# Kernel optimization log

Hardware: AMD Instinct MI355X
Metric: run time of the kernel (lower is better)

Reference implementation:

```python
import jax, jax.numpy as jnp
import numpy as np

N = 100000      # nodes
E = 6400000     # edges
F_IN = 128      # input feature dim (lazily inferred by PyG)
C = 2           # out_channels (hard-coded in module)
NEG_SLOPE = 0.2 # GATConv default leaky_relu slope


def setup_inputs() -> dict:
    key = jax.random.key(0)
    ks = jax.random.split(key, 8)
    x = jax.random.normal(ks[0], (N, F_IN), dtype=jnp.float32)
    edge_index = jax.random.randint(ks[1], (2, E), 0, N, dtype=jnp.int64)
    edge_attr = jax.random.normal(ks[2], (E, 1), dtype=jnp.float32)
    s = 1.0 / np.sqrt(F_IN)
    W_src = (jax.random.normal(ks[3], (F_IN, C), dtype=jnp.float32) * s)
    W_edge = jax.random.normal(ks[4], (1, C), dtype=jnp.float32)
    att_src = jax.random.normal(ks[5], (C,), dtype=jnp.float32)
    att_dst = jax.random.normal(ks[6], (C,), dtype=jnp.float32)
    att_edge = jax.random.normal(ks[7], (C,), dtype=jnp.float32)
    bias = jnp.zeros((C,), dtype=jnp.float32)
    return {"x": x, "edge_index": edge_index, "edge_attr": edge_attr,
            "W_src": W_src, "W_edge": W_edge, "att_src": att_src,
            "att_dst": att_dst, "att_edge": att_edge, "bias": bias}


def reference(x, edge_index, edge_attr, W_src, W_edge, att_src, att_dst, att_edge, bias):
    src, dst = edge_index[0], edge_index[1]
    # Single-tensor input in PyG GATConv -> x_src = x_dst = lin_src(x)
    h = x @ W_src                      # [N, C]  (heads=1 folded away)
    a_src = h @ att_src                # [N]
    a_dst = h @ att_dst                # [N]
    he = edge_attr @ W_edge            # [E, C]
    a_e = he @ att_edge                # [E]
    # per-edge attention logit
    alpha = a_src[src] + a_dst[dst] + a_e
    alpha = jax.nn.leaky_relu(alpha, NEG_SLOPE)
    # segment softmax over incoming edges of each destination node
    amax = jax.ops.segment_max(alpha, dst, num_segments=N)
    amax = jnp.where(jnp.isfinite(amax), amax, 0.0)  # empty segments
    ex = jnp.exp(alpha - amax[dst])
    denom = jax.ops.segment_sum(ex, dst, num_segments=N)
    alpha_n = ex / (denom[dst] + 1e-16)
    # weighted scatter-add aggregation
    msg = h[src] * alpha_n[:, None]    # [E, C]
    out = jax.ops.segment_sum(msg, dst, num_segments=N) + bias  # [N, C]
    return out, alpha_n[:, None]       # alpha: [E, heads=1]
```

## Files before the change

### kernel.cpp

```cpp
#include <hip/hip_runtime.h>
#include <hip/hip_fp16.h>

#define NN 100000
#define NE 6400000
#define NEG_SLOPE 0.2f

#define NBIN 32
#define BSLICE 3125
#define NCH 16
#define ABLK 512
#define EPB (NE / ABLK)
#define RND 4096
#define CAP 256
#define SROW 257
#define NODEBLK 1024

#define FSLICE 10240
#define FNSLICE 10
#define FNCHUNK 20
#define FCHUNK (NE / FNCHUNK)

__global__ void gat_node_hist(const float* __restrict__ x, const float* __restrict__ W,
                              const float* __restrict__ att_src, const float* __restrict__ att_dst,
                              uint2* __restrict__ pack8, float* __restrict__ asrc,
                              float* __restrict__ adst,
                              const int* __restrict__ dst, int* __restrict__ cnt) {
    if (blockIdx.x < NODEBLK) {
        int gtid = blockIdx.x * 256 + threadIdx.x;
        int wave = gtid >> 6, lane = threadIdx.x & 63;
        const int nw = (NODEBLK * 256) >> 6;
        float as0 = att_src[0], as1 = att_src[1];
        float ad0 = att_dst[0], ad1 = att_dst[1];
        for (int node = wave; node < NN; node += nw) {
            float2 xx = *(const float2*)(x + (size_t)node * 128 + lane * 2);
            float2 w0 = *(const float2*)(W + lane * 4);
            float2 w1 = *(const float2*)(W + lane * 4 + 2);
            float c0 = xx.x * w0.x + xx.y * w1.x;
            float c1 = xx.x * w0.y + xx.y * w1.y;
            #pragma unroll
            for (int off = 32; off; off >>= 1) {
                c0 += __shfl_down(c0, off);
                c1 += __shfl_down(c1, off);
            }
            if (lane == 0) {
                float s = c0 * as0 + c1 * as1;
                float d = c0 * ad0 + c1 * ad1;
                unsigned h01 = (unsigned)__half_as_ushort(__float2half_rn(c0)) |
                               ((unsigned)__half_as_ushort(__float2half_rn(c1)) << 16);
                pack8[node] = make_uint2(h01, __float_as_uint(s));
                asrc[node] = s;
                adst[node] = d;
            }
        }
    } else {
        __shared__ unsigned h[NBIN];
        const int ablk = blockIdx.x - NODEBLK, t = threadIdx.x;
        if (t < NBIN) h[t] = 0;
        __syncthreads();
        const int b0 = ablk * EPB;
        for (int o = t * 4; o < EPB; o += 1024) {
            int4 d4 = *(const int4*)(dst + b0 + o);
            const int* dp = (const int*)&d4;
            #pragma unroll
            for (int u = 0; u < 4; ++u)
                atomicAdd(&h[(unsigned)dp[u] / BSLICE], 1u);
        }
        __syncthreads();
        if (t < NBIN) cnt[t * ABLK + ablk] = (int)h[t];
    }
}

__global__ __launch_bounds__(1024) void
gat_prefix(int* __restrict__ cnt, int* __restrict__ binstart) {
    __shared__ int btot[NBIN];
    __shared__ int bst[NBIN + 1];
    const int t = threadIdx.x, w = t >> 6, l = t & 63;
    int c[2][8], s[2], incl[2];
    #pragma unroll
    for (int q = 0; q < 2; ++q) {
        const int b = w + q * 16;
        int* row = cnt + b * ABLK;
        int ss = 0;
        #pragma unroll
        for (int j = 0; j < 8; ++j) { c[q][j] = row[l * 8 + j]; ss += c[q][j]; }
        int inc = ss;
        #pragma unroll
        for (int d = 1; d < 64; d <<= 1) {
            int v = __shfl_up(inc, d);
            if (l >= d) inc += v;
        }
        if (l == 63) btot[b] = inc;
        s[q] = ss; incl[q] = inc;
    }
    __syncthreads();
    if (t == 0) {
        int run = 0;
        for (int b = 0; b < NBIN; ++b) { bst[b] = run; run += btot[b]; }
        bst[NBIN] = run;
    }
    __syncthreads();
    #pragma unroll
    for (int q = 0; q < 2; ++q) {
        const int b = w + q * 16;
        int* row = cnt + b * ABLK;
        int base = bst[b] + incl[q] - s[q];
        #pragma unroll
        for (int j = 0; j < 8; ++j) { row[l * 8 + j] = base; base += c[q][j]; }
    }
    if (t <= NBIN) binstart[t] = bst[t];
}

__global__ __launch_bounds__(1024) void
gat_scatter(const int* __restrict__ src, const int* __restrict__ dst,
            const float* __restrict__ ea, const uint2* __restrict__ pack8,
            const float* __restrict__ adst,
            const float* __restrict__ W_edge, const float* __restrict__ att_edge,
            const int* __restrict__ base, uint2* __restrict__ recs,
            __half* __restrict__ elog) {
    __shared__ uint2 stage[NBIN * SROW];
    __shared__ unsigned cur[NBIN], flushed[NBIN], bbase[NBIN];
    const int ablk = blockIdx.x, t = threadIdx.x;
    if (t < NBIN) {
        cur[t] = 0; flushed[t] = 0;
        bbase[t] = (unsigned)base[t * ABLK + ablk];
    }
    __syncthreads();
    const float k = W_edge[0] * att_edge[0] + W_edge[1] * att_edge[1];
    const int b0 = ablk * EPB;
    const int nrounds = (EPB + RND - 1) / RND;

    for (int r = 0; r < nrounds; ++r) {
        const int lim = EPB - r * RND;
        const bool act = (t * 4) < lim;
        const int o = act ? (r * RND + t * 4) : 0;
        const int i = b0 + o;
        int4 s4 = *(const int4*)(src + i);
        int4 d4 = *(const int4*)(dst + i);
        float4 e4 = *(const float4*)(ea + i);
        const int* sp = (const int*)&s4;
        const int* dp = (const int*)&d4;
        const float* ep = (const float*)&e4;
        uint2 ps[4];
        float ad[4];
        #pragma unroll
        for (int u = 0; u < 4; ++u) {
            ps[u] = pack8[sp[u]];
            ad[u] = adst[dp[u]];
        }
        float al[4];
        #pragma unroll
        for (int u = 0; u < 4; ++u) {
            float a = __uint_as_float(ps[u].y) + ad[u] + k * ep[u];
            al[u] = a > 0.0f ? a : NEG_SLOPE * a;
        }
        if (act) {
            if (elog) {
                uint2 ev;
                ev.x = (unsigned)__half_as_ushort(__float2half_rn(al[0])) |
                       ((unsigned)__half_as_ushort(__float2half_rn(al[1])) << 16);
                ev.y = (unsigned)__half_as_ushort(__float2half_rn(al[2])) |
                       ((unsigned)__half_as_ushort(__float2half_rn(al[3])) << 16);
                *(uint2*)(elog + i) = ev;
            }
            #pragma unroll
            for (int u = 0; u < 4; ++u) {
                unsigned d = (unsigned)dp[u];
                unsigned bin = d / BSLICE;
                unsigned off = d - bin * BSLICE;
                unsigned pos = atomicAdd(&cur[bin], 1u);
                unsigned lo = (unsigned)__half_as_ushort(__float2half_rn(al[u])) | (off << 16);
                stage[bin * SROW + (pos & (CAP - 1))] = make_uint2(ps[u].x, lo);
            }
        }
        __syncthreads();
        const int w = t >> 6, l = t & 63;
        const bool last = (r == nrounds - 1);
        for (int b = w * 2; b < w * 2 + 2; ++b) {
            unsigned start = flushed[b];
            unsigned n = cur[b] - start;
            if (!last) n &= ~15u;
            if (n) {
                size_t gb = (size_t)bbase[b] + start;
                for (unsigned j = l; j < n; j += 64)
                    recs[gb + j] = stage[b * SROW + ((start + j) & (CAP - 1))];
                if (l == 0) flushed[b] = start + n;
            }
        }
        __syncthreads();
    }
}

__global__ __launch_bounds__(1024) void
gat_scan(const uint2* __restrict__ recs, const int* __restrict__ binstart,
         float* __restrict__ partial) {
    __shared__ float   dacc[BSLICE];
    __shared__ __half2 hacc[BSLICE];
    const int blk = blockIdx.x, t = threadIdx.x;
    const int b = blk / NCH, c = blk % NCH;
    for (int j = t; j < BSLICE; j += 1024) {
        dacc[j] = 0.f;
        hacc[j] = __floats2half2_rn(0.f, 0.f);
    }
    __syncthreads();
    const int s0 = binstart[b], len = binstart[b + 1] - s0;
    const int c0 = s0 + (int)((long long)len * c / NCH);
    const int c1 = s0 + (int)((long long)len * (c + 1) / NCH);

#define PROC(r)                                                                \
    do {                                                                       \
        unsigned off_ = (r).y >> 16;                                           \
        float al_ = __half2float(__ushort_as_half((unsigned short)((r).y & 0xFFFFu))); \
        float ex_ = __expf(al_);                                               \
        float h0_ = __half2float(__ushort_as_half((unsigned short)((r).x & 0xFFFFu))); \
        float h1_ = __half2float(__ushort_as_half((unsigned short)((r).x >> 16)));     \
        atomicAdd(&dacc[off_], ex_);                                           \
        unsafeAtomicAdd(&hacc[off_], __floats2half2_rn(ex_ * h0_, ex_ * h1_)); \
    } while (0)

    int i = c0 + t;
    for (; i + 7 * 1024 < c1; i += 8 * 1024) {
        uint2 r0 = recs[i],          r1 = recs[i + 1024];
        uint2 r2 = recs[i + 2048],   r3 = recs[i + 3072];
        uint2 r4 = recs[i + 4096],   r5 = recs[i + 5120];
        uint2 r6 = recs[i + 6144],   r7 = recs[i + 7168];
        PROC(r0); PROC(r1); PROC(r2); PROC(r3);
        PROC(r4); PROC(r5); PROC(r6); PROC(r7);
    }
    for (; i < c1; i += 1024) {
        uint2 r = recs[i];
        PROC(r);
    }
#undef PROC
    __syncthreads();
    float* p = partial + (size_t)blk * (2 * BSLICE);
    unsigned* pu = (unsigned*)(p + BSLICE);
    const unsigned* hb = (const unsigned*)hacc;
    for (int j = t; j < BSLICE; j += 1024) {
        p[j] = dacc[j];
        pu[j] = hb[j];
    }
}

__global__ void gat_combine(const float* __restrict__ partial,
                            const float* __restrict__ bias,
                            float* __restrict__ out, float* __restrict__ invd) {
    int n = blockIdx.x * blockDim.x + threadIdx.x;
    if (n >= NN) return;
    int b = n / BSLICE, off = n % BSLICE;
    const float* pbase = partial + (size_t)(b * NCH) * (2 * BSLICE);
    float de = 0.f, n0 = 0.f, n1 = 0.f;
    for (int c = 0; c < NCH; ++c) {
        const float* p = pbase + (size_t)c * (2 * BSLICE);
        de += p[off];
        unsigned hb = ((const unsigned*)p)[BSLICE + off];
        float2 hf = __half22float2(*(const __half2*)&hb);
        n0 += hf.x; n1 += hf.y;
    }
    float inv = 1.0f / (de + 1e-16f);
    out[2 * n]     = n0 * inv + bias[0];
    out[2 * n + 1] = n1 * inv + bias[1];
    invd[n] = inv;
}

__global__ void gat_alpha_fast(const int* __restrict__ dst, const __half* __restrict__ elog,
                               const float* __restrict__ invd, float* __restrict__ alpha) {
    int i = (blockIdx.x * blockDim.x + threadIdx.x) * 4;
    if (i >= NE) return;
    int4 d4 = *(const int4*)(dst + i);
    uint2 ev = *(const uint2*)(elog + i);
    const int* dp = (const int*)&d4;
    float iv[4];
    #pragma unroll
    for (int u = 0; u < 4; ++u) iv[u] = invd[dp[u]];
    float al[4] = {
        __half2float(__ushort_as_half((unsigned short)(ev.x & 0xFFFFu))),
        __half2float(__ushort_as_half((unsigned short)(ev.x >> 16))),
        __half2float(__ushort_as_half((unsigned short)(ev.y & 0xFFFFu))),
        __half2float(__ushort_as_half((unsigned short)(ev.y >> 16)))};
    float4 a;
    float* ap = (float*)&a;
    #pragma unroll
    for (int u = 0; u < 4; ++u) ap[u] = __expf(al[u]) * iv[u];
    *(float4*)(alpha + i) = a;
}

__global__ void gat_alpha(const int* __restrict__ src, const int* __restrict__ dst,
                          const float* __restrict__ ea,
                          const float* __restrict__ asrc, const float* __restrict__ adst,
                          const float* __restrict__ invd,
                          const float* __restrict__ W_edge, const float* __restrict__ att_edge,
                          float* __restrict__ alpha) {
    const float k = W_edge[0] * att_edge[0] + W_edge[1] * att_edge[1];
    int i = (blockIdx.x * blockDim.x + threadIdx.x) * 4;
    if (i >= NE) return;
    int4   d4 = *(const int4*)(dst + i);
    int4   s4 = *(const int4*)(src + i);
    float4 e4 = *(const float4*)(ea + i);
    const int*   dp = (const int*)&d4;
    const int*   sp = (const int*)&s4;
    const float* ep = (const float*)&e4;
    float as[4], ad[4], iv[4];
    #pragma unroll
    for (int u = 0; u < 4; ++u) {
        as[u] = asrc[sp[u]];
        ad[u] = adst[dp[u]];
        iv[u] = invd[dp[u]];
    }
    float4 a;
    float* ap = (float*)&a;
    #pragma unroll
    for (int u = 0; u < 4; ++u) {
        float al = as[u] + ad[u] + k * ep[u];
        al = al > 0.0f ? al : NEG_SLOPE * al;
        ap[u] = __expf(al) * iv[u];
    }
    *(float4*)(alpha + i) = a;
}

__global__ void gat_node_fb(const float* __restrict__ x, const float* __restrict__ W,
                            const float* __restrict__ att_src, const float* __restrict__ att_dst,
                            float4* __restrict__ pack, float* __restrict__ asrc,
                            float* __restrict__ adst, int n) {
    int gtid = blockIdx.x * blockDim.x + threadIdx.x;
    int wave = gtid >> 6, lane = threadIdx.x & 63;
    int nw = (gridDim.x * blockDim.x) >> 6;
    float as0 = att_src[0], as1 = att_src[1];
    float ad0 = att_dst[0], ad1 = att_dst[1];
    for (int node = wave; node < n; node += nw) {
        float2 xx = *(const float2*)(x + (size_t)node * 128 + lane * 2);
        float2 w0 = *(const float2*)(W + lane * 4);
        float2 w1 = *(const float2*)(W + lane * 4 + 2);
        float c0 = xx.x * w0.x + xx.y * w1.x;
        float c1 = xx.x * w0.y + xx.y * w1.y;
        #pragma unroll
        for (int off = 32; off; off >>= 1) {
            c0 += __shfl_down(c0, off);
            c1 += __shfl_down(c1, off);
        }
        if (lane == 0) {
            float s = c0 * as0 + c1 * as1;
            float d = c0 * ad0 + c1 * ad1;
            pack[node] = make_float4(c0, c1, s, d);
            asrc[node] = s;
            adst[node] = d;
        }
    }
}

__global__ __launch_bounds__(1024) void
gat_scan_fb(const int* __restrict__ src, const int* __restrict__ dst,
            const float* __restrict__ ea, const float4* __restrict__ pack,
            const float* __restrict__ adst,
            const float* __restrict__ W_edge, const float* __restrict__ att_edge,
            float* __restrict__ partial) {
    __shared__ float sacc[FSLICE * 3];
    const int s = blockIdx.x / FNCHUNK;
    const int c = blockIdx.x % FNCHUNK;
    const int lo = s * FSLICE;
    for (int j = threadIdx.x; j < FSLICE * 3; j += 1024) sacc[j] = 0.0f;
    __syncthreads();
    const float k = W_edge[0] * att_edge[0] + W_edge[1] * att_edge[1];
    const int base = c * FCHUNK;
    for (int o = threadIdx.x * 8; o < FCHUNK; o += 1024 * 8) {
        const int i = base + o;
        int4   da = *(const int4*)(dst + i), db = *(const int4*)(dst + i + 4);
        int4   sa = *(const int4*)(src + i), sb = *(const int4*)(src + i + 4);
        float4 e0 = *(const float4*)(ea + i), e1 = *(const float4*)(ea + i + 4);
        int   dd[8] = {da.x, da.y, da.z, da.w, db.x, db.y, db.z, db.w};
        int   ss[8] = {sa.x, sa.y, sa.z, sa.w, sb.x, sb.y, sb.z, sb.w};
        float ee[8] = {e0.x, e0.y, e0.z, e0.w, e1.x, e1.y, e1.z, e1.w};
        unsigned off[8];
        float4 ps[8];
        float  ad[8];
        #pragma unroll
        for (int u = 0; u < 8; ++u) {
            off[u] = (unsigned)(dd[u] - lo);
            bool acc = off[u] < FSLICE;
            ps[u] = pack[acc ? ss[u] : 0];
            ad[u] = adst[acc ? dd[u] : lo];
        }
        #pragma unroll
        for (int u = 0; u < 8; ++u) {
            float al = ps[u].z + ad[u] + k * ee[u];
            al = al > 0.0f ? al : NEG_SLOPE * al;
            float ex = __expf(al);
            if (off[u] < FSLICE) {
                atomicAdd(&sacc[off[u] * 3],     ex);
                atomicAdd(&sacc[off[u] * 3 + 1], ex * ps[u].x);
                atomicAdd(&sacc[off[u] * 3 + 2], ex * ps[u].y);
            }
        }
    }
    __syncthreads();
    float* pout = partial + (size_t)blockIdx.x * (FSLICE * 3);
    for (int j = threadIdx.x; j < FSLICE * 3; j += 1024) pout[j] = sacc[j];
}

__global__ void gat_combine_fb(const float* __restrict__ partial,
                               const float* __restrict__ bias,
                               float* __restrict__ out, float* __restrict__ invd) {
    int n = blockIdx.x * blockDim.x + threadIdx.x;
    if (n >= NN) return;
    int sl = n / FSLICE, off = n % FSLICE;
    const float* p = partial + (size_t)sl * FNCHUNK * (FSLICE * 3) + (size_t)off * 3;
    float de = 0.f, n0 = 0.f, n1 = 0.f;
    for (int c = 0; c < FNCHUNK; ++c, p += FSLICE * 3) {
        de += p[0]; n0 += p[1]; n1 += p[2];
    }
    float inv = 1.0f / (de + 1e-16f);
    out[2 * n]     = n0 * inv + bias[0];
    out[2 * n + 1] = n1 * inv + bias[1];
    invd[n] = inv;
}

extern "C" void kernel_launch(void* const* d_in, const int* in_sizes, int n_in,
                              void* d_out, int out_size, void* d_ws, size_t ws_size,
                              hipStream_t stream) {
    const float* x        = (const float*)d_in[0];
    const int*   ei       = (const int*)  d_in[1];
    const float* ea       = (const float*)d_in[2];
    const float* W_src    = (const float*)d_in[3];
    const float* W_edge   = (const float*)d_in[4];
    const float* att_src  = (const float*)d_in[5];
    const float* att_dst  = (const float*)d_in[6];
    const float* att_edge = (const float*)d_in[7];
    const float* bias     = (const float*)d_in[8];

    float* out   = (float*)d_out;
    float* alpha = out + 2 * NN;

    const int* src = ei;
    const int* dst = ei + NE;

    size_t fixed = (size_t)NE * 8 + (size_t)NN * 8 + 3 * (size_t)NN * 4
                 + (size_t)NBIN * ABLK * 4 + (NBIN + 1) * 4 + 512;
    size_t need_mid  = fixed;
    size_t need_fast = fixed + (size_t)NE * 2;

    if (ws_size >= need_mid) {
        uint2*  recs = (uint2*)d_ws;
        uint2*  pack8 = (uint2*)((char*)d_ws + (size_t)NE * 8);
        float*  asrc = (float*)(pack8 + NN);
        float*  adst = asrc + NN;
        float*  invd = adst + NN;
        int*    cnt  = (int*)(invd + NN);
        int*    binstart = cnt + NBIN * ABLK;
        __half* elog = nullptr;
        if (ws_size >= need_fast) {
            uintptr_t p = ((uintptr_t)(binstart + NBIN + 1) + 255) & ~(uintptr_t)255;
            elog = (__half*)p;
        }
        float*  partial = alpha;

        gat_node_hist<<<NODEBLK + ABLK, 256, 0, stream>>>(x, W_src, att_src, att_dst,
                                                          pack8, asrc, adst, dst, cnt);
        gat_prefix  <<<1, 1024, 0, stream>>>(cnt, binstart);
        gat_scatter <<<ABLK, 1024, 0, stream>>>(src, dst, ea, pack8, adst,
                                                W_edge, att_edge, cnt, recs, elog);
        gat_scan    <<<NBIN * NCH, 1024, 0, stream>>>(recs, binstart, partial);
        gat_combine <<<(NN + 255) / 256, 256, 0, stream>>>(partial, bias, out, invd);
        if (elog)
            gat_alpha_fast<<<NE / (256 * 4), 256, 0, stream>>>(dst, elog, invd, alpha);
        else
            gat_alpha<<<NE / (256 * 4), 256, 0, stream>>>(src, dst, ea, asrc, adst, invd,
                                                          W_edge, att_edge, alpha);
    } else {
        float4* pack = (float4*)d_ws;
        float*  asrc = (float*)(pack + NN);
        float*  adst = asrc + NN;
        float*  invd = adst + NN;
        float*  partial = alpha;

        gat_node_fb   <<<1024, 256, 0, stream>>>(x, W_src, att_src, att_dst, pack, asrc, adst, NN);
        gat_scan_fb   <<<FNSLICE * FNCHUNK, 1024, 0, stream>>>(src, dst, ea, pack, adst,
                                                               W_edge, att_edge, partial);
        gat_combine_fb<<<(NN + 255) / 256, 256, 0, stream>>>(partial, bias, out, invd);
        gat_alpha     <<<NE / (256 * 4), 256, 0, stream>>>(src, dst, ea, asrc, adst, invd,
                                                           W_edge, att_edge, alpha);
    }
}
```

Measured before the change: 194.6 us.

## Defer a_dst gather to bin scan via shared memory and prefetch scatter inputs

The scatter kernel no longer gathers adst per edge. It stores only the partial logit (a_src + edge term), and the scan kernel adds a_dst from a per-bin shared-memory copy before applying leaky ReLU, removing one random global gather per edge. The scatter loop also software-prefetches the next round's src/dst/ea vectors to overlap loads with the staging work. The combine kernel now writes a packed float2 of (adst, inv) so the alpha kernels fetch both with one gather, at the cost of extra shared memory in the scan kernel and slightly more ALU work there.

```diff
diff --git a/kernel.cpp b/kernel.cpp
--- a/kernel.cpp
+++ b/kernel.cpp
@@ -113,7 +113,6 @@
 __global__ __launch_bounds__(1024) void
 gat_scatter(const int* __restrict__ src, const int* __restrict__ dst,
             const float* __restrict__ ea, const uint2* __restrict__ pack8,
-            const float* __restrict__ adst,
             const float* __restrict__ W_edge, const float* __restrict__ att_edge,
             const int* __restrict__ base, uint2* __restrict__ recs,
             __half* __restrict__ elog) {
@@ -129,37 +128,40 @@
     const int b0 = ablk * EPB;
     const int nrounds = (EPB + RND - 1) / RND;
 
+    int4 s4 = *(const int4*)(src + b0 + t * 4);
+    int4 d4 = *(const int4*)(dst + b0 + t * 4);
+    float4 e4 = *(const float4*)(ea + b0 + t * 4);
+
     for (int r = 0; r < nrounds; ++r) {
         const int lim = EPB - r * RND;
         const bool act = (t * 4) < lim;
-        const int o = act ? (r * RND + t * 4) : 0;
-        const int i = b0 + o;
-        int4 s4 = *(const int4*)(src + i);
-        int4 d4 = *(const int4*)(dst + i);
-        float4 e4 = *(const float4*)(ea + i);
+        const int i = b0 + (act ? (r * RND + t * 4) : 0);
         const int* sp = (const int*)&s4;
         const int* dp = (const int*)&d4;
         const float* ep = (const float*)&e4;
         uint2 ps[4];
-        float ad[4];
-        #pragma unroll
-        for (int u = 0; u < 4; ++u) {
+        #pragma unroll
+        for (int u = 0; u < 4; ++u)
             ps[u] = pack8[sp[u]];
-            ad[u] = adst[dp[u]];
-        }
-        float al[4];
-        #pragma unroll
-        for (int u = 0; u < 4; ++u) {
-            float a = __uint_as_float(ps[u].y) + ad[u] + k * ep[u];
-            al[u] = a > 0.0f ? a : NEG_SLOPE * a;
-        }
+        int4 ns4, nd4; float4 ne4;
+        if (r + 1 < nrounds) {
+            const int no = b0 + (((t * 4) < (EPB - (r + 1) * RND))
+                                 ? ((r + 1) * RND + t * 4) : 0);
+            ns4 = *(const int4*)(src + no);
+            nd4 = *(const int4*)(dst + no);
+            ne4 = *(const float4*)(ea + no);
+        }
+        float pl[4];
+        #pragma unroll
+        for (int u = 0; u < 4; ++u)
+            pl[u] = __uint_as_float(ps[u].y) + k * ep[u];
         if (act) {
             if (elog) {
                 uint2 ev;
-                ev.x = (unsigned)__half_as_ushort(__float2half_rn(al[0])) |
-                       ((unsigned)__half_as_ushort(__float2half_rn(al[1])) << 16);
-                ev.y = (unsigned)__half_as_ushort(__float2half_rn(al[2])) |
-                       ((unsigned)__half_as_ushort(__float2half_rn(al[3])) << 16);
+                ev.x = (unsigned)__half_as_ushort(__float2half_rn(pl[0])) |
+                       ((unsigned)__half_as_ushort(__float2half_rn(pl[1])) << 16);
+                ev.y = (unsigned)__half_as_ushort(__float2half_rn(pl[2])) |
+                       ((unsigned)__half_as_ushort(__float2half_rn(pl[3])) << 16);
                 *(uint2*)(elog + i) = ev;
             }
             #pragma unroll
@@ -168,7 +170,7 @@
                 unsigned bin = d / BSLICE;
                 unsigned off = d - bin * BSLICE;
                 unsigned pos = atomicAdd(&cur[bin], 1u);
-                unsigned lo = (unsigned)__half_as_ushort(__float2half_rn(al[u])) | (off << 16);
+                unsigned lo = (unsigned)__half_as_ushort(__float2half_rn(pl[u])) | (off << 16);
                 stage[bin * SROW + (pos & (CAP - 1))] = make_uint2(ps[u].x, lo);
             }
         }
@@ -187,19 +189,22 @@
             }
         }
         __syncthreads();
+        s4 = ns4; d4 = nd4; e4 = ne4;
     }
 }
 
 __global__ __launch_bounds__(1024) void
 gat_scan(const uint2* __restrict__ recs, const int* __restrict__ binstart,
-         float* __restrict__ partial) {
+         const float* __restrict__ adst, float* __restrict__ partial) {
     __shared__ float   dacc[BSLICE];
     __shared__ __half2 hacc[BSLICE];
+    __shared__ float   sadst[BSLICE];
     const int blk = blockIdx.x, t = threadIdx.x;
     const int b = blk / NCH, c = blk % NCH;
     for (int j = t; j < BSLICE; j += 1024) {
         dacc[j] = 0.f;
         hacc[j] = __floats2half2_rn(0.f, 0.f);
+        sadst[j] = adst[b * BSLICE + j];
     }
     __syncthreads();
     const int s0 = binstart[b], len = binstart[b + 1] - s0;
@@ -209,7 +214,9 @@
 #define PROC(r)                                                                \
     do {                                                                       \
         unsigned off_ = (r).y >> 16;                                           \
-        float al_ = __half2float(__ushort_as_half((unsigned short)((r).y & 0xFFFFu))); \
+        float al_ = __half2float(__ushort_as_half((unsigned short)((r).y & 0xFFFFu))) \
+                  + sadst[off_];                                               \
+        al_ = al_ > 0.f ? al_ : NEG_SLOPE * al_;                               \
         float ex_ = __expf(al_);                                               \
         float h0_ = __half2float(__ushort_as_half((unsigned short)((r).x & 0xFFFFu))); \
         float h1_ = __half2float(__ushort_as_half((unsigned short)((r).x >> 16)));     \
@@ -242,8 +249,9 @@
 }
 
 __global__ void gat_combine(const float* __restrict__ partial,
+                            const float* __restrict__ adst,
                             const float* __restrict__ bias,
-                            float* __restrict__ out, float* __restrict__ invd) {
+                            float* __restrict__ out, float2* __restrict__ adiv) {
     int n = blockIdx.x * blockDim.x + threadIdx.x;
     if (n >= NN) return;
     int b = n / BSLICE, off = n % BSLICE;
@@ -259,20 +267,20 @@
     float inv = 1.0f / (de + 1e-16f);
     out[2 * n]     = n0 * inv + bias[0];
     out[2 * n + 1] = n1 * inv + bias[1];
-    invd[n] = inv;
+    adiv[n] = make_float2(adst[n], inv);
 }
 
 __global__ void gat_alpha_fast(const int* __restrict__ dst, const __half* __restrict__ elog,
-                               const float* __restrict__ invd, float* __restrict__ alpha) {
+                               const float2* __restrict__ adiv, float* __restrict__ alpha) {
     int i = (blockIdx.x * blockDim.x + threadIdx.x) * 4;
     if (i >= NE) return;
     int4 d4 = *(const int4*)(dst + i);
     uint2 ev = *(const uint2*)(elog + i);
     const int* dp = (const int*)&d4;
-    float iv[4];
-    #pragma unroll
-    for (int u = 0; u < 4; ++u) iv[u] = invd[dp[u]];
-    float al[4] = {
+    float2 av[4];
+    #pragma unroll
+    for (int u = 0; u < 4; ++u) av[u] = adiv[dp[u]];
+    float pl[4] = {
         __half2float(__ushort_as_half((unsigned short)(ev.x & 0xFFFFu))),
         __half2float(__ushort_as_half((unsigned short)(ev.x >> 16))),
         __half2float(__ushort_as_half((unsigned short)(ev.y & 0xFFFFu))),
@@ -280,16 +288,19 @@
     float4 a;
     float* ap = (float*)&a;
     #pragma unroll
-    for (int u = 0; u < 4; ++u) ap[u] = __expf(al[u]) * iv[u];
+    for (int u = 0; u < 4; ++u) {
+        float al = pl[u] + av[u].x;
+        al = al > 0.0f ? al : NEG_SLOPE * al;
+        ap[u] = __expf(al) * av[u].y;
+    }
     *(float4*)(alpha + i) = a;
 }
 
-__global__ void gat_alpha(const int* __restrict__ src, const int* __restrict__ dst,
-                          const float* __restrict__ ea,
-                          const float* __restrict__ asrc, const float* __restrict__ adst,
-                          const float* __restrict__ invd,
-                          const float* __restrict__ W_edge, const float* __restrict__ att_edge,
-                          float* __restrict__ alpha) {
+__global__ void gat_alpha_mid(const int* __restrict__ src, const int* __restrict__ dst,
+                              const float* __restrict__ ea,
+                              const float* __restrict__ asrc, const float2* __restrict__ adiv,
+                              const float* __restrict__ W_edge, const float* __restrict__ att_edge,
+                              float* __restrict__ alpha) {
     const float k = W_edge[0] * att_edge[0] + W_edge[1] * att_edge[1];
     int i = (blockIdx.x * blockDim.x + threadIdx.x) * 4;
     if (i >= NE) return;
@@ -299,20 +310,20 @@
     const int*   dp = (const int*)&d4;
     const int*   sp = (const int*)&s4;
     const float* ep = (const float*)&e4;
-    float as[4], ad[4], iv[4];
+    float  as[4];
+    float2 av[4];
     #pragma unroll
     for (int u = 0; u < 4; ++u) {
         as[u] = asrc[sp[u]];
-        ad[u] = adst[dp[u]];
-        iv[u] = invd[dp[u]];
+        av[u] = adiv[dp[u]];
     }
     float4 a;
     float* ap = (float*)&a;
     #pragma unroll
     for (int u = 0; u < 4; ++u) {
-        float al = as[u] + ad[u] + k * ep[u];
+        float al = as[u] + av[u].x + k * ep[u];
         al = al > 0.0f ? al : NEG_SLOPE * al;
-        ap[u] = __expf(al) * iv[u];
+        ap[u] = __expf(al) * av[u].y;
     }
     *(float4*)(alpha + i) = a;
 }
@@ -397,8 +408,9 @@
 }
 
 __global__ void gat_combine_fb(const float* __restrict__ partial,
+                               const float* __restrict__ adst,
                                const float* __restrict__ bias,
-                               float* __restrict__ out, float* __restrict__ invd) {
+                               float* __restrict__ out, float2* __restrict__ adiv) {
     int n = blockIdx.x * blockDim.x + threadIdx.x;
     if (n >= NN) return;
     int sl = n / FSLICE, off = n % FSLICE;
@@ -410,7 +422,7 @@
     float inv = 1.0f / (de + 1e-16f);
     out[2 * n]     = n0 * inv + bias[0];
     out[2 * n + 1] = n1 * inv + bias[1];
-    invd[n] = inv;
+    adiv[n] = make_float2(adst[n], inv);
 }
 
 extern "C" void kernel_launch(void* const* d_in, const int* in_sizes, int n_in,
@@ -432,20 +444,21 @@
     const int* src = ei;
     const int* dst = ei + NE;
 
-    size_t fixed = (size_t)NE * 8 + (size_t)NN * 8 + 3 * (size_t)NN * 4
-                 + (size_t)NBIN * ABLK * 4 + (NBIN + 1) * 4 + 512;
+    size_t fixed = (size_t)NE * 8 + (size_t)NN * 8 + 2 * (size_t)NN * 4
+                 + (size_t)NN * 8 + (size_t)NBIN * ABLK * 4
+                 + (NBIN + 1) * 4 + 512;
     size_t need_mid  = fixed;
     size_t need_fast = fixed + (size_t)NE * 2;
 
     if (ws_size >= need_mid) {
-        uint2*  recs = (uint2*)d_ws;
+        uint2*  recs  = (uint2*)d_ws;
         uint2*  pack8 = (uint2*)((char*)d_ws + (size_t)NE * 8);
-        float*  asrc = (float*)(pack8 + NN);
-        float*  adst = asrc + NN;
-        float*  invd = adst + NN;
-        int*    cnt  = (int*)(invd + NN);
+        float*  asrc  = (float*)(pack8 + NN);
+        float*  adst  = asrc + NN;
+        float2* adiv  = (float2*)(adst + NN);
+        int*    cnt   = (int*)(adiv + NN);
         int*    binstart = cnt + NBIN * ABLK;
-        __half* elog = nullptr;
+        __half* elog  = nullptr;
         if (ws_size >= need_fast) {
             uintptr_t p = ((uintptr_t)(binstart + NBIN + 1) + 255) & ~(uintptr_t)255;
             elog = (__half*)p;
@@ -455,27 +468,27 @@
         gat_node_hist<<<NODEBLK + ABLK, 256, 0, stream>>>(x, W_src, att_src, att_dst,
                                                           pack8, asrc, adst, dst, cnt);
         gat_prefix  <<<1, 1024, 0, stream>>>(cnt, binstart);
-        gat_scatter <<<ABLK, 1024, 0, stream>>>(src, dst, ea, pack8, adst,
+        gat_scatter <<<ABLK, 1024, 0, stream>>>(src, dst, ea, pack8,
                                                 W_edge, att_edge, cnt, recs, elog);
-        gat_scan    <<<NBIN * NCH, 1024, 0, stream>>>(recs, binstart, partial);
-        gat_combine <<<(NN + 255) / 256, 256, 0, stream>>>(partial, bias, out, invd);
+        gat_scan    <<<NBIN * NCH, 1024, 0, stream>>>(recs, binstart, adst, partial);
+        gat_combine <<<(NN + 255) / 256, 256, 0, stream>>>(partial, adst, bias, out, adiv);
         if (elog)
-            gat_alpha_fast<<<NE / (256 * 4), 256, 0, stream>>>(dst, elog, invd, alpha);
+            gat_alpha_fast<<<NE / (256 * 4), 256, 0, stream>>>(dst, elog, adiv, alpha);
         else
-            gat_alpha<<<NE / (256 * 4), 256, 0, stream>>>(src, dst, ea, asrc, adst, invd,
-                                                          W_edge, att_edge, alpha);
+            gat_alpha_mid<<<NE / (256 * 4), 256, 0, stream>>>(src, dst, ea, asrc, adiv,
+                                                              W_edge, att_edge, alpha);
     } else {
         float4* pack = (float4*)d_ws;
         float*  asrc = (float*)(pack + NN);
         float*  adst = asrc + NN;
-        float*  invd = adst + NN;
+        float2* adiv = (float2*)(adst + NN);
         float*  partial = alpha;
 
         gat_node_fb   <<<1024, 256, 0, stream>>>(x, W_src, att_src, att_dst, pack, asrc, adst, NN);
         gat_scan_fb   <<<FNSLICE * FNCHUNK, 1024, 0, stream>>>(src, dst, ea, pack, adst,
                                                                W_edge, att_edge, partial);
-        gat_combine_fb<<<(NN + 255) / 256, 256, 0, stream>>>(partial, bias, out, invd);
-        gat_alpha     <<<NE / (256 * 4), 256, 0, stream>>>(src, dst, ea, asrc, adst, invd,
+        gat_combine_fb<<<(NN + 255) / 256, 256, 0, stream>>>(partial, adst, bias, out, adiv);
+        gat_alpha_mid <<<NE / (256 * 4), 256, 0, stream>>>(src, dst, ea, asrc, adiv,
                                                            W_edge, att_edge, alpha);
     }
 }
```

Measured after the change: 171.7 us. -11.8%, faster.
